# Kernel optimization log

Measured on AMD Instinct MI355X. Metric: run time of the kernel, lower is better.

The kernel has to match this reference:

```python
import jax, jax.numpy as jnp
import numpy as np

E = 512   # embed_dim
H = 8     # num_heads
DH = E // H  # head_dim = 64
L = 1024  # tgt_len (language tokens)
S = 1024  # src_len (video/audio tokens)
B = 8     # batch
EPS = 1e-8


def setup_inputs() -> dict:
    key = jax.random.key(0)
    ks = jax.random.split(key, 12)
    xavier = float(np.sqrt(2.0 / (E + E)))
    inp = {
        "query": jax.random.normal(ks[0], (L, B, E), jnp.float32),
        "mod1": jax.random.normal(ks[1], (S, B, E), jnp.float32),
        "mod2": jax.random.normal(ks[2], (S, B, E), jnp.float32),
    }
    wnames = ["Wq", "Wk1", "Wk2", "Wv1", "Wv2", "Wg1", "Wg2", "Wo"]
    for i, n in enumerate(wnames):
        inp[n] = jax.random.normal(ks[3 + i], (E, E), jnp.float32) * xavier
        inp["b" + n[1:]] = jnp.zeros((E,), jnp.float32)
    return inp


def _heads(x):
    # (T, B, E) -> (B*H, T, DH), fairseq-style head split
    T = x.shape[0]
    return x.reshape(T, B * H, DH).transpose(1, 0, 2)


def reference(query, mod1, mod2,
              Wq, bq, Wk1, bk1, Wk2, bk2,
              Wv1, bv1, Wv2, bv2,
              Wg1, bg1, Wg2, bg2, Wo, bo):
    scaling = DH ** -0.5
    q = (query @ Wq.T + bq) * scaling          # (L, B, E)
    k1 = mod1 @ Wk1.T + bk1                    # (S, B, E)
    k2 = mod2 @ Wk2.T + bk2
    # gated values: v_i * sigmoid(gate_i(mod_i)), summed across modalities
    v = ((mod1 @ Wv1.T + bv1) * jax.nn.sigmoid(mod1 @ Wg1.T + bg1)
         + (mod2 @ Wv2.T + bv2) * jax.nn.sigmoid(mod2 @ Wg2.T + bg2))

    qh, k1h, k2h, vh = _heads(q), _heads(k1), _heads(k2), _heads(v)  # (B*H, T, DH)

    # 3x3 Gram determinant scores (computed via GEMMs, no [B,L,S,D] broadcast)
    ll = jnp.sum(qh * qh, -1)[:, :, None]        # (BH, L, 1)
    vv = jnp.sum(k1h * k1h, -1)[:, None, :]      # (BH, 1, S)
    aa = jnp.sum(k2h * k2h, -1)[:, None, :]
    va = jnp.sum(k1h * k2h, -1)[:, None, :]
    lv = jnp.einsum('bld,bsd->bls', qh, k1h)     # (BH, L, S)
    la = jnp.einsum('bld,bsd->bls', qh, k2h)
    det = (ll * (vv * aa - va * va)
           - lv * (lv * aa - la * va)
           + la * (lv * va - la * vv))
    scores = -jnp.sqrt(jnp.clip(det, EPS))       # (BH, L, S)

    attn = jax.nn.softmax(scores, axis=-1)
    out = jnp.einsum('bls,bsd->bld', attn, vh)   # (BH, L, DH)
    out = out.transpose(1, 0, 2).reshape(L, B, E)
    return out @ Wo.T + bo                       # (L, B, E)
```

## Files before the change

kernel.cpp:

```cpp
#include <hip/hip_runtime.h>
#include <math.h>


typedef short bf16x8 __attribute__((ext_vector_type(8)));
typedef float f32x4  __attribute__((ext_vector_type(4)));

#define MFMA16(a,b,c) __builtin_amdgcn_mfma_f32_16x16x32_bf16((a),(b),(c),0,0,0)

static constexpr float LOG2E_F = 1.4426950408889634f;
static constexpr float CBRT_L2E = 1.12994722f;
static constexpr float DEFER_THR = 11.54156033f;
static constexpr float EPS_SCALED = 2.0813689e-8f;

typedef const __attribute__((address_space(1))) unsigned int gas_u32;
typedef __attribute__((address_space(3))) unsigned int las_u32;

__device__ __forceinline__ void gload16(const void* g, void* l){
  __builtin_amdgcn_global_load_lds((gas_u32*)g, (las_u32*)l, 16, 0, 0);
}

__device__ __forceinline__ float b2f(unsigned short s){
  union { unsigned u; float f; } v; v.u = ((unsigned)s) << 16; return v.f;
}
__device__ __forceinline__ unsigned short f2b(float f){
  union { float f; unsigned u; } v; v.f = f;
  unsigned r = v.u + 0x7fffu + ((v.u >> 16) & 1u);
  return (unsigned short)(r >> 16);
}

__global__ __launch_bounds__(256) void split3_kernel(
    const float* __restrict__ a, const float* __restrict__ b,
    const float* __restrict__ c,
    unsigned short* __restrict__ hi, unsigned short* __restrict__ lo, int n)
{
  const int y = blockIdx.y;
  const float* src = (y == 0) ? a : ((y == 1) ? b : c);
  unsigned short* h = hi + (size_t)y * n;
  unsigned short* L = lo + (size_t)y * n;
  int stride = gridDim.x * 256;
  for (int i = blockIdx.x*256 + threadIdx.x; i < n; i += stride){
    float v = src[i];
    unsigned short hh = f2b(v);
    h[i] = hh;
    L[i] = f2b(v - b2f(hh));
  }
}

__global__ __launch_bounds__(256) void splitW_kernel(
    const float* w0, const float* w1, const float* w2, const float* w3,
    const float* w4, const float* w5, const float* w6, const float* w7,
    unsigned short* __restrict__ hi, unsigned short* __restrict__ lo, int n)
{
  const int y = blockIdx.y;
  const float* src = w0;
  if (y == 1) src = w1; if (y == 2) src = w2; if (y == 3) src = w3;
  if (y == 4) src = w4; if (y == 5) src = w5; if (y == 6) src = w6;
  if (y == 7) src = w7;
  unsigned short* h = hi + (size_t)y * n;
  unsigned short* L = lo + (size_t)y * n;
  int stride = gridDim.x * 256;
  for (int i = blockIdx.x*256 + threadIdx.x; i < n; i += stride){
    float v = src[i];
    unsigned short hh = f2b(v);
    h[i] = hh;
    L[i] = f2b(v - b2f(hh));
  }
}

__global__ __launch_bounds__(256,2) void proj_kernel(
    const unsigned short* __restrict__ xhi, const unsigned short* __restrict__ xlo,
    const unsigned short* __restrict__ whi, const unsigned short* __restrict__ wlo,
    const float* __restrict__ bq, const float* __restrict__ bk1,
    const float* __restrict__ bk2,
    const float* __restrict__ bv1, const float* __restrict__ bg1,
    const float* __restrict__ bv2, const float* __restrict__ bg2,
    unsigned short* __restrict__ qh_hi, unsigned short* __restrict__ qh_lo,
    unsigned short* __restrict__ k1h_hi, unsigned short* __restrict__ k1h_lo,
    unsigned short* __restrict__ k2h_hi, unsigned short* __restrict__ k2h_lo,
    float* __restrict__ vacc1, float* __restrict__ vacc2)
{
  __shared__ unsigned short smem[2*4*4096];
  const int tid = threadIdx.x, w = tid >> 6, l = tid & 63;
  const int y = blockIdx.y;
  const int job = y >> 2;
  const int r0 = blockIdx.x * 128, e0 = (y & 3) * 128;
  const int lrow = l & 15, kg = l >> 4;
  const bool isGate = (job >= 3);

  const size_t NXs = (size_t)8192*512, NWs = (size_t)512*512;
  const int aidx = (job == 0) ? 0 : ((job == 1 || job == 3) ? 1 : 2);
  const unsigned short* Ahi = xhi + (size_t)aidx * NXs;
  const unsigned short* Alo = xlo + (size_t)aidx * NXs;
  const int bidx = isGate ? ((job == 3) ? 3 : 4) : job;
  const unsigned short* Bhi = whi + (size_t)bidx * NWs;
  const unsigned short* Blo = wlo + (size_t)bidx * NWs;
  const unsigned short* Bg  = whi + (size_t)((job == 3) ? 5 : 6) * NWs;

  f32x4 acc[4][4], gacc[4][4];
  #pragma unroll
  for (int m = 0; m < 4; ++m)
    #pragma unroll
    for (int n = 0; n < 4; ++n){
      acc[m][n] = (f32x4){0.f,0.f,0.f,0.f};
      gacc[m][n] = (f32x4){0.f,0.f,0.f,0.f};
    }

  const int sgsw = ((l & 3) ^ ((l >> 3) & 3)) * 8;
  const int srA = r0 + w*16 + (l >> 2);
  const int srB = e0 + w*16 + (l >> 2);

  auto stage = [&](int buf, int kk){
    const int lb = buf*4*4096 + w*512;
    #pragma unroll
    for (int j = 0; j < 2; ++j){
      const size_t ga = (size_t)(srA + j*64)*512 + kk + sgsw;
      const size_t gb = (size_t)(srB + j*64)*512 + kk + sgsw;
      gload16(&Ahi[ga], &smem[lb + 0*4096 + j*2048]);
      if (!isGate) gload16(&Alo[ga], &smem[lb + 1*4096 + j*2048]);
      else         gload16(&Bg[gb],  &smem[lb + 1*4096 + j*2048]);
      gload16(&Bhi[gb], &smem[lb + 2*4096 + j*2048]);
      gload16(&Blo[gb], &smem[lb + 3*4096 + j*2048]);
    }
  };

  const int rowA = (w >> 1)*64 + lrow;
  const int rowB = (w & 1)*64 + lrow;
  const int kgs  = (kg ^ ((lrow >> 1) & 3)) * 8;

  auto compute = [&](int buf){
    const int bb = buf*4*4096;
    bf16x8 ah[4], al[4];
    #pragma unroll
    for (int m = 0; m < 4; ++m){
      const int ra = (rowA + m*16)*32 + kgs;
      ah[m] = *(const bf16x8*)&smem[bb + ra];
      if (!isGate) al[m] = *(const bf16x8*)&smem[bb + 4096 + ra];
    }
    #pragma unroll
    for (int n = 0; n < 4; ++n){
      const int rb = (rowB + n*16)*32 + kgs;
      bf16x8 bh = *(const bf16x8*)&smem[bb + 8192 + rb];
      bf16x8 bl = *(const bf16x8*)&smem[bb + 12288 + rb];
      #pragma unroll
      for (int m = 0; m < 4; ++m){
        acc[m][n] = MFMA16(ah[m], bh, acc[m][n]);
        acc[m][n] = MFMA16(ah[m], bl, acc[m][n]);
      }
      if (!isGate){
        #pragma unroll
        for (int m = 0; m < 4; ++m)
          acc[m][n] = MFMA16(al[m], bh, acc[m][n]);
      } else {
        bf16x8 bg = *(const bf16x8*)&smem[bb + 4096 + rb];
        #pragma unroll
        for (int m = 0; m < 4; ++m)
          gacc[m][n] = MFMA16(ah[m], bg, gacc[m][n]);
      }
    }
  };

  stage(0, 0);
  __syncthreads();
  for (int t = 0; t < 16; ++t){
    if (t < 15) stage((t+1) & 1, (t+1)*32);
    compute(t & 1);
    __syncthreads();
  }

  if (!isGate){
    const float* bias = (job == 0) ? bq : ((job == 1) ? bk1 : bk2);
    const float scale = (job == 0) ? 0.125f*CBRT_L2E : CBRT_L2E;
    unsigned short* oH = (job == 0) ? qh_hi : ((job == 1) ? k1h_hi : k2h_hi);
    unsigned short* oL = (job == 0) ? qh_lo : ((job == 1) ? k1h_lo : k2h_lo);
    #pragma unroll
    for (int n = 0; n < 4; ++n){
      const int e = e0 + (w & 1)*64 + n*16 + lrow;
      const float bv = bias[e];
      #pragma unroll
      for (int m = 0; m < 4; ++m){
        #pragma unroll
        for (int q = 0; q < 4; ++q){
          const int r = r0 + (w >> 1)*64 + m*16 + kg*4 + q;
          const float yv = (acc[m][n][q] + bv) * scale;
          const int bh = ((r & 7) << 3) + (e >> 6);
          const size_t off = ((size_t)bh*1024 + (r >> 3))*64 + (e & 63);
          unsigned short hh = f2b(yv);
          oH[off] = hh;
          oL[off] = f2b(yv - b2f(hh));
        }
      }
    }
  } else {
    const float* bvv = (job == 3) ? bv1 : bv2;
    const float* bgg = (job == 3) ? bg1 : bg2;
    float* outF = (job == 3) ? vacc1 : vacc2;
    #pragma unroll
    for (int n = 0; n < 4; ++n){
      const int e = e0 + (w & 1)*64 + n*16 + lrow;
      const float bv = bvv[e], bg_ = bgg[e];
      #pragma unroll
      for (int m = 0; m < 4; ++m){
        #pragma unroll
        for (int q = 0; q < 4; ++q){
          const int r = r0 + (w >> 1)*64 + m*16 + kg*4 + q;
          const float yv = acc[m][n][q] + bv;
          const float yg = gacc[m][n][q] + bg_;
          const float sg = 1.0f / (1.0f + exp2f(-yg * LOG2E_F));
          outF[(size_t)r*512 + e] = yv * sg;
        }
      }
    }
  }
}

__global__ __launch_bounds__(256,2) void gemmout_kernel(
    const unsigned short* __restrict__ Ahi,
    const unsigned short* __restrict__ Bhi, const unsigned short* __restrict__ Blo,
    const float* __restrict__ bias, float* __restrict__ outF)
{
  __shared__ unsigned short smem[2*10240];
  const int tid = threadIdx.x, w = tid >> 6, l = tid & 63;
  const int r0 = blockIdx.x * 64, e0 = blockIdx.y * 128;
  const int lrow = l & 15, kg = l >> 4;

  f32x4 acc[2][4];
  #pragma unroll
  for (int m = 0; m < 2; ++m)
    #pragma unroll
    for (int n = 0; n < 4; ++n) acc[m][n] = (f32x4){0.f,0.f,0.f,0.f};

  const int sgsw = ((l & 3) ^ ((l >> 3) & 3)) * 8;
  const int srA = r0 + w*16 + (l >> 2);
  const int srB = e0 + w*16 + (l >> 2);

  auto stage = [&](int buf, int kk){
    const int lb = buf*10240;
    gload16(&Ahi[(size_t)srA*512 + kk + sgsw], &smem[lb + tid*8]);
    #pragma unroll
    for (int j = 0; j < 2; ++j){
      const size_t gb = (size_t)(srB + j*64)*512 + kk + sgsw;
      gload16(&Bhi[gb], &smem[lb + 2048 + (tid + j*256)*8]);
      gload16(&Blo[gb], &smem[lb + 6144 + (tid + j*256)*8]);
    }
  };

  const int rowA = (w >> 1)*32 + lrow;
  const int rowB = (w & 1)*64 + lrow;
  const int kgs  = (kg ^ ((lrow >> 1) & 3)) * 8;

  auto compute = [&](int buf){
    const int bb = buf*10240;
    bf16x8 ah[2];
    #pragma unroll
    for (int m = 0; m < 2; ++m)
      ah[m] = *(const bf16x8*)&smem[bb + (rowA + m*16)*32 + kgs];
    #pragma unroll
    for (int n = 0; n < 4; ++n){
      const int rb = (rowB + n*16)*32 + kgs;
      bf16x8 bh = *(const bf16x8*)&smem[bb + 2048 + rb];
      bf16x8 bl = *(const bf16x8*)&smem[bb + 6144 + rb];
      #pragma unroll
      for (int m = 0; m < 2; ++m){
        acc[m][n] = MFMA16(ah[m], bh, acc[m][n]);
        acc[m][n] = MFMA16(ah[m], bl, acc[m][n]);
      }
    }
  };

  stage(0, 0);
  __syncthreads();
  for (int t = 0; t < 16; ++t){
    if (t < 15) stage((t+1) & 1, (t+1)*32);
    compute(t & 1);
    __syncthreads();
  }

  #pragma unroll
  for (int n = 0; n < 4; ++n){
    const int e = e0 + (w & 1)*64 + n*16 + lrow;
    const float bv = bias[e];
    #pragma unroll
    for (int m = 0; m < 2; ++m){
      #pragma unroll
      for (int q = 0; q < 4; ++q){
        const int r = r0 + (w >> 1)*32 + m*16 + kg*4 + q;
        outF[(size_t)r*512 + e] = acc[m][n][q] + bv;
      }
    }
  }
}

__global__ __launch_bounds__(256) void norms_kernel(
    const unsigned short* __restrict__ qh, const unsigned short* __restrict__ ql,
    const unsigned short* __restrict__ k1h, const unsigned short* __restrict__ k1l,
    const unsigned short* __restrict__ k2h, const unsigned short* __restrict__ k2l,
    float* __restrict__ ll, f32x4* __restrict__ nrm4)
{
  const int idx = blockIdx.x*256 + threadIdx.x;
  const size_t base = (size_t)idx * 64;
  float sll = 0.f, svv = 0.f, saa = 0.f, sva = 0.f;
  #pragma unroll
  for (int j = 0; j < 8; ++j){
    bf16x8 q_h = *(const bf16x8*)&qh[base + j*8];
    bf16x8 q_l = *(const bf16x8*)&ql[base + j*8];
    bf16x8 a_h = *(const bf16x8*)&k1h[base + j*8];
    bf16x8 a_l = *(const bf16x8*)&k1l[base + j*8];
    bf16x8 c_h = *(const bf16x8*)&k2h[base + j*8];
    bf16x8 c_l = *(const bf16x8*)&k2l[base + j*8];
    #pragma unroll
    for (int i = 0; i < 8; ++i){
      float qv = b2f((unsigned short)q_h[i]) + b2f((unsigned short)q_l[i]);
      float a1 = b2f((unsigned short)a_h[i]) + b2f((unsigned short)a_l[i]);
      float a2 = b2f((unsigned short)c_h[i]) + b2f((unsigned short)c_l[i]);
      sll += qv*qv; svv += a1*a1; saa += a2*a2; sva += a1*a2;
    }
  }
  ll[idx] = sll;
  nrm4[idx] = (f32x4){svv*saa - sva*sva, saa, 2.0f*sva, svv};
}

__global__ __launch_bounds__(256) void vtrans_kernel(
    const float* __restrict__ v1, const float* __restrict__ v2,
    unsigned short* __restrict__ vTh)
{
  __shared__ unsigned short sH[64*64];
  const int bh = blockIdx.y, b = bh >> 3, h = bh & 7;
  const int s0 = blockIdx.x * 64;
  const int tid = threadIdx.x;
  for (int c = tid; c < 1024; c += 256){
    const int i = c >> 4, sl = c & 15;
    const size_t g = ((size_t)(s0 + i)*8 + b)*512 + h*64 + sl*4;
    f32x4 a = *(const f32x4*)&v1[g];
    f32x4 bb = *(const f32x4*)&v2[g];
    #pragma unroll
    for (int e = 0; e < 4; ++e)
      sH[(sl*4 + e)*64 + i] = f2b(a[e] + bb[e]);
  }
  __syncthreads();
  for (int c = tid; c < 512; c += 256){
    const int d = c >> 3, sl = c & 7;
    const size_t g = ((size_t)bh*64 + d)*1024 + s0 + sl*8;
    *(bf16x8*)&vTh[g] = *(const bf16x8*)&sH[d*64 + sl*8];
  }
}

__global__ __launch_bounds__(256,2) void attn_kernel(
    const unsigned short* __restrict__ qhh, const unsigned short* __restrict__ qhl,
    const unsigned short* __restrict__ k1hh, const unsigned short* __restrict__ k1hl,
    const unsigned short* __restrict__ k2hh, const unsigned short* __restrict__ k2hl,
    const unsigned short* __restrict__ vTh,
    const float* __restrict__ llv, const f32x4* __restrict__ nrm4,
    unsigned short* __restrict__ aoHi)
{
  __shared__ unsigned short sK1h[4096];
  __shared__ unsigned short sK1l[4096];
  __shared__ unsigned short sK2h[4096];
  __shared__ unsigned short sK2l[4096];
  __shared__ unsigned short sVh[4096];
  __shared__ unsigned short sPh[8192];
  __shared__ f32x4 sN4[64];

  const int bh = blockIdx.x & 63, l0 = (blockIdx.x >> 6) * 128;
  const int tid = threadIdx.x, w = tid >> 6, lane = tid & 63;
  const int lrow = lane & 15, kg = lane >> 4;

  bf16x8 qfh[2][2], qfl[2][2];
  #pragma unroll
  for (int m = 0; m < 2; ++m){
    const size_t qb = ((size_t)bh*1024 + l0 + w*32 + m*16 + lrow)*64 + kg*8;
    qfh[m][0] = *(const bf16x8*)&qhh[qb];
    qfl[m][0] = *(const bf16x8*)&qhl[qb];
    qfh[m][1] = *(const bf16x8*)&qhh[qb + 32];
    qfl[m][1] = *(const bf16x8*)&qhl[qb + 32];
  }
  float ll_r[2][4];
  #pragma unroll
  for (int m = 0; m < 2; ++m)
    #pragma unroll
    for (int q = 0; q < 4; ++q)
      ll_r[m][q] = llv[bh*1024 + l0 + w*32 + m*16 + kg*4 + q];

  f32x4 accO[2][4];
  #pragma unroll
  for (int m = 0; m < 2; ++m)
    #pragma unroll
    for (int i = 0; i < 4; ++i) accO[m][i] = (f32x4){0.f,0.f,0.f,0.f};
  float mn[2][4], s_run[2][4];
  #pragma unroll
  for (int m = 0; m < 2; ++m)
    #pragma unroll
    for (int q = 0; q < 4; ++q){ mn[m][q] = 1e30f; s_run[m][q] = 0.f; }

  const int c0 = tid, c1 = tid + 256;
  const int r0g = c0 >> 3, g0 = ((c0 & 7) ^ (r0g & 7)) * 8;
  const int r1g = c1 >> 3, g1 = ((c1 & 7) ^ (r1g & 7)) * 8;

  for (int ss = 0; ss < 1024; ss += 64){
    {
      const size_t kb = (size_t)bh*1024 + ss;
      const size_t k0 = (kb + r0g)*64 + g0;
      const size_t k1_ = (kb + r1g)*64 + g1;
      gload16(&k1hh[k0], &sK1h[c0*8]);  gload16(&k1hh[k1_], &sK1h[c1*8]);
      gload16(&k1hl[k0], &sK1l[c0*8]);  gload16(&k1hl[k1_], &sK1l[c1*8]);
      gload16(&k2hh[k0], &sK2h[c0*8]);  gload16(&k2hh[k1_], &sK2h[c1*8]);
      gload16(&k2hl[k0], &sK2l[c0*8]);  gload16(&k2hl[k1_], &sK2l[c1*8]);
      const size_t v0 = ((size_t)bh*64 + r0g)*1024 + ss + g0;
      const size_t v1 = ((size_t)bh*64 + r1g)*1024 + ss + g1;
      gload16(&vTh[v0], &sVh[c0*8]);    gload16(&vTh[v1], &sVh[c1*8]);
      if (tid < 64) gload16(&nrm4[(size_t)bh*1024 + ss + tid], &sN4[tid]);
    }
    __syncthreads();

    float p_[2][4][4];
    float tmn[2][4];
    #pragma unroll
    for (int m = 0; m < 2; ++m)
      #pragma unroll
      for (int q = 0; q < 4; ++q) tmn[m][q] = 1e30f;

    #pragma unroll
    for (int nt = 0; nt < 4; ++nt){
      f32x4 lv[2], la[2];
      #pragma unroll
      for (int m = 0; m < 2; ++m){ lv[m] = (f32x4){0.f,0.f,0.f,0.f}; la[m] = (f32x4){0.f,0.f,0.f,0.f}; }
      #pragma unroll
      for (int ks = 0; ks < 2; ++ks){
        const int row = nt*16 + lrow;
        const int off = row*64 + (((ks*4 + kg) ^ (row & 7)) * 8);
        bf16x8 b1h = *(const bf16x8*)&sK1h[off];
        bf16x8 b1l = *(const bf16x8*)&sK1l[off];
        bf16x8 b2h = *(const bf16x8*)&sK2h[off];
        bf16x8 b2l = *(const bf16x8*)&sK2l[off];
        #pragma unroll
        for (int m = 0; m < 2; ++m){
          lv[m] = MFMA16(qfh[m][ks], b1h, lv[m]);
          lv[m] = MFMA16(qfh[m][ks], b1l, lv[m]);
          lv[m] = MFMA16(qfl[m][ks], b1h, lv[m]);
          la[m] = MFMA16(qfh[m][ks], b2h, la[m]);
          la[m] = MFMA16(qfh[m][ks], b2l, la[m]);
          la[m] = MFMA16(qfl[m][ks], b2h, la[m]);
        }
      }
      f32x4 n4 = sN4[nt*16 + lrow];
      const float cross = n4[0], c_aa = n4[1], c_va2 = n4[2], c_vv = n4[3];
      #pragma unroll
      for (int m = 0; m < 2; ++m){
        #pragma unroll
        for (int q = 0; q < 4; ++q){
          const float flv = lv[m][q], fla = la[m][q];
          float t = fmaf(-c_vv, fla*fla, (flv*fla)*c_va2);
          t = fmaf(-c_aa, flv*flv, t);
          const float det = fmaf(ll_r[m][q], cross, t);
          const float sq = __builtin_amdgcn_sqrtf(fmaxf(det, EPS_SCALED));
          p_[m][nt][q] = sq;
          tmn[m][q] = fminf(tmn[m][q], sq);
        }
      }
    }
    #pragma unroll
    for (int m = 0; m < 2; ++m)
      #pragma unroll
      for (int q = 0; q < 4; ++q){
        tmn[m][q] = fminf(tmn[m][q], __shfl_xor(tmn[m][q], 1));
        tmn[m][q] = fminf(tmn[m][q], __shfl_xor(tmn[m][q], 2));
        tmn[m][q] = fminf(tmn[m][q], __shfl_xor(tmn[m][q], 4));
        tmn[m][q] = fminf(tmn[m][q], __shfl_xor(tmn[m][q], 8));
      }
    int up = 0;
    #pragma unroll
    for (int m = 0; m < 2; ++m)
      #pragma unroll
      for (int q = 0; q < 4; ++q) up |= (tmn[m][q] < mn[m][q] - DEFER_THR) ? 1 : 0;
    if (__any(up)){
      #pragma unroll
      for (int m = 0; m < 2; ++m)
        #pragma unroll
        for (int q = 0; q < 4; ++q){
          const float mnn = fminf(mn[m][q], tmn[m][q]);
          const float rs = __builtin_amdgcn_exp2f(mnn - mn[m][q]);
          mn[m][q] = mnn;
          s_run[m][q] *= rs;
          #pragma unroll
          for (int dt = 0; dt < 4; ++dt) accO[m][dt][q] *= rs;
        }
    }
    float ps[2][4];
    #pragma unroll
    for (int m = 0; m < 2; ++m)
      #pragma unroll
      for (int q = 0; q < 4; ++q) ps[m][q] = 0.f;
    #pragma unroll
    for (int nt = 0; nt < 4; ++nt)
      #pragma unroll
      for (int m = 0; m < 2; ++m)
        #pragma unroll
        for (int q = 0; q < 4; ++q){
          const float e = __builtin_amdgcn_exp2f(mn[m][q] - p_[m][nt][q]);
          p_[m][nt][q] = e;
          ps[m][q] += e;
        }
    #pragma unroll
    for (int m = 0; m < 2; ++m)
      #pragma unroll
      for (int q = 0; q < 4; ++q){
        float v = ps[m][q];
        v += __shfl_xor(v, 1); v += __shfl_xor(v, 2);
        v += __shfl_xor(v, 4); v += __shfl_xor(v, 8);
        s_run[m][q] += v;
      }

    #pragma unroll
    for (int m = 0; m < 2; ++m){
      #pragma unroll
      for (int nt = 0; nt < 4; ++nt){
        const int col = nt*16 + lrow;
        const int cg = col >> 3, cr = col & 7;
        #pragma unroll
        for (int qp = 0; qp < 2; ++qp){
          unsigned int pk;
          asm("v_cvt_pk_bf16_f32 %0, %1, %2" : "=v"(pk)
              : "v"(p_[m][nt][qp*2]), "v"(p_[m][nt][qp*2+1]));
          const int ra = m*16 + kg*4 + qp*2, rb = ra + 1;
          sPh[w*2048 + ra*64 + ((cg ^ (ra & 7))*8) + cr] = (unsigned short)(pk & 0xffffu);
          sPh[w*2048 + rb*64 + ((cg ^ (rb & 7))*8) + cr] = (unsigned short)(pk >> 16);
        }
      }
    }

    #pragma unroll
    for (int ks = 0; ks < 2; ++ks){
      bf16x8 pa[2];
      #pragma unroll
      for (int m = 0; m < 2; ++m){
        const int prow = m*16 + lrow;
        pa[m] = *(const bf16x8*)&sPh[w*2048 + prow*64 + (((ks*4 + kg) ^ (prow & 7))*8)];
      }
      #pragma unroll
      for (int dt = 0; dt < 4; ++dt){
        const int vrow = dt*16 + lrow;
        bf16x8 bvh = *(const bf16x8*)&sVh[vrow*64 + (((ks*4 + kg) ^ (vrow & 7))*8)];
        #pragma unroll
        for (int m = 0; m < 2; ++m)
          accO[m][dt] = MFMA16(pa[m], bvh, accO[m][dt]);
      }
    }
    __syncthreads();
  }

  const int b = bh >> 3, h = bh & 7;
  #pragma unroll
  for (int m = 0; m < 2; ++m){
    float rcp[4];
    #pragma unroll
    for (int q = 0; q < 4; ++q) rcp[q] = __builtin_amdgcn_rcpf(s_run[m][q]);
    #pragma unroll
    for (int dt = 0; dt < 4; ++dt){
      const int d = dt*16 + lrow;
      #pragma unroll
      for (int q = 0; q < 4; ++q){
        const int l_ = l0 + w*32 + m*16 + kg*4 + q;
        aoHi[((size_t)l_*8 + b)*512 + h*64 + d] = f2b(accO[m][dt][q] * rcp[q]);
      }
    }
  }
}

extern "C" void kernel_launch(void* const* d_in, const int* in_sizes, int n_in,
                              void* d_out, int out_size, void* d_ws, size_t ws_size,
                              hipStream_t stream)
{
  const float* query = (const float*)d_in[0];
  const float* mod1  = (const float*)d_in[1];
  const float* mod2  = (const float*)d_in[2];
  const float* bq  = (const float*)d_in[4];
  const float* bk1 = (const float*)d_in[6];
  const float* bk2 = (const float*)d_in[8];
  const float* bv1 = (const float*)d_in[10];
  const float* bv2 = (const float*)d_in[12];
  const float* bg1 = (const float*)d_in[14];
  const float* bg2 = (const float*)d_in[16];
  const float* bo  = (const float*)d_in[18];

  char* p = (char*)d_ws;
  auto take = [&](size_t bytes) -> char* {
    char* r = p; p += (bytes + 255) & ~(size_t)255; return r;
  };
  const size_t NX = (size_t)8192*512;
  const size_t NW = (size_t)512*512;
  const size_t XB = NX*2, WB = NW*2;
  const size_t HB = (size_t)64*1024*64*2;
  const size_t FB = NX*4;
  const size_t NB = (size_t)64*1024*4;

  unsigned short* xhi = (unsigned short*)take(3*XB);
  unsigned short* xlo = (unsigned short*)take(3*XB);
  unsigned short* whi = (unsigned short*)take(8*WB);
  unsigned short* wlo = (unsigned short*)take(8*WB);
  unsigned short* qh_hi  = (unsigned short*)take(HB);
  unsigned short* qh_lo  = (unsigned short*)take(HB);
  unsigned short* k1h_hi = (unsigned short*)take(HB);
  unsigned short* k1h_lo = (unsigned short*)take(HB);
  unsigned short* k2h_hi = (unsigned short*)take(HB);
  unsigned short* k2h_lo = (unsigned short*)take(HB);
  unsigned short* vT_hi  = (unsigned short*)take(HB);
  float* vacc1 = (float*)take(FB);
  float* vacc2 = (float*)take(FB);
  unsigned short* ao_hi = (unsigned short*)take(HB);
  float* llv = (float*)take(NB);
  f32x4* nrm4 = (f32x4*)take(4*NB);

  split3_kernel<<<dim3(1024,3), 256, 0, stream>>>(query, mod1, mod2, xhi, xlo, (int)NX);
  splitW_kernel<<<dim3(256,8), 256, 0, stream>>>(
      (const float*)d_in[3], (const float*)d_in[5], (const float*)d_in[7],
      (const float*)d_in[9], (const float*)d_in[11], (const float*)d_in[13],
      (const float*)d_in[15], (const float*)d_in[17], whi, wlo, (int)NW);

  proj_kernel<<<dim3(64, 20), 256, 0, stream>>>(
      xhi, xlo, whi, wlo, bq, bk1, bk2, bv1, bg1, bv2, bg2,
      qh_hi, qh_lo, k1h_hi, k1h_lo, k2h_hi, k2h_lo, vacc1, vacc2);

  norms_kernel<<<256, 256, 0, stream>>>(qh_hi, qh_lo, k1h_hi, k1h_lo,
                                        k2h_hi, k2h_lo, llv, nrm4);
  vtrans_kernel<<<dim3(16, 64), 256, 0, stream>>>(vacc1, vacc2, vT_hi);

  attn_kernel<<<512, 256, 0, stream>>>(
      qh_hi, qh_lo, k1h_hi, k1h_lo, k2h_hi, k2h_lo, vT_hi,
      llv, nrm4, ao_hi);

  gemmout_kernel<<<dim3(128, 4), 256, 0, stream>>>(
      ao_hi, whi + 7*NW, wlo + 7*NW, bo, (float*)d_out);
}
```

Measured before the change: 371.0 us.

## Drop activation lo-split in projections, split QK/VG kernels, raise MFMA priority

```diff
diff --git a/kernel.cpp b/kernel.cpp
--- a/kernel.cpp
+++ b/kernel.cpp
@@ -28,21 +28,25 @@
   return (unsigned short)(r >> 16);
 }
 
-__global__ __launch_bounds__(256) void split3_kernel(
+__global__ __launch_bounds__(256) void cast3_kernel(
     const float* __restrict__ a, const float* __restrict__ b,
-    const float* __restrict__ c,
-    unsigned short* __restrict__ hi, unsigned short* __restrict__ lo, int n)
+    const float* __restrict__ c, unsigned short* __restrict__ hi, int n)
 {
   const int y = blockIdx.y;
   const float* src = (y == 0) ? a : ((y == 1) ? b : c);
   unsigned short* h = hi + (size_t)y * n;
-  unsigned short* L = lo + (size_t)y * n;
+  const int n8 = n >> 3;
   int stride = gridDim.x * 256;
-  for (int i = blockIdx.x*256 + threadIdx.x; i < n; i += stride){
-    float v = src[i];
-    unsigned short hh = f2b(v);
-    h[i] = hh;
-    L[i] = f2b(v - b2f(hh));
+  for (int i = blockIdx.x*256 + threadIdx.x; i < n8; i += stride){
+    f32x4 v0 = *(const f32x4*)&src[i*8];
+    f32x4 v1 = *(const f32x4*)&src[i*8 + 4];
+    bf16x8 o;
+    #pragma unroll
+    for (int j = 0; j < 4; ++j){
+      o[j]   = (short)f2b(v0[j]);
+      o[j+4] = (short)f2b(v1[j]);
+    }
+    *(bf16x8*)&h[i*8] = o;
   }
 }
 
@@ -67,59 +71,45 @@
   }
 }
 
-__global__ __launch_bounds__(256,2) void proj_kernel(
-    const unsigned short* __restrict__ xhi, const unsigned short* __restrict__ xlo,
+__global__ __launch_bounds__(256,3) void proj_qk_kernel(
+    const unsigned short* __restrict__ xhi,
     const unsigned short* __restrict__ whi, const unsigned short* __restrict__ wlo,
     const float* __restrict__ bq, const float* __restrict__ bk1,
     const float* __restrict__ bk2,
-    const float* __restrict__ bv1, const float* __restrict__ bg1,
-    const float* __restrict__ bv2, const float* __restrict__ bg2,
     unsigned short* __restrict__ qh_hi, unsigned short* __restrict__ qh_lo,
     unsigned short* __restrict__ k1h_hi, unsigned short* __restrict__ k1h_lo,
-    unsigned short* __restrict__ k2h_hi, unsigned short* __restrict__ k2h_lo,
-    float* __restrict__ vacc1, float* __restrict__ vacc2)
-{
-  __shared__ unsigned short smem[2*4*4096];
+    unsigned short* __restrict__ k2h_hi, unsigned short* __restrict__ k2h_lo)
+{
+  __shared__ unsigned short smem[2*3*4096];
   const int tid = threadIdx.x, w = tid >> 6, l = tid & 63;
-  const int y = blockIdx.y;
-  const int job = y >> 2;
+  const int y = blockIdx.y, job = y >> 2;
   const int r0 = blockIdx.x * 128, e0 = (y & 3) * 128;
   const int lrow = l & 15, kg = l >> 4;
-  const bool isGate = (job >= 3);
 
   const size_t NXs = (size_t)8192*512, NWs = (size_t)512*512;
-  const int aidx = (job == 0) ? 0 : ((job == 1 || job == 3) ? 1 : 2);
-  const unsigned short* Ahi = xhi + (size_t)aidx * NXs;
-  const unsigned short* Alo = xlo + (size_t)aidx * NXs;
-  const int bidx = isGate ? ((job == 3) ? 3 : 4) : job;
-  const unsigned short* Bhi = whi + (size_t)bidx * NWs;
-  const unsigned short* Blo = wlo + (size_t)bidx * NWs;
-  const unsigned short* Bg  = whi + (size_t)((job == 3) ? 5 : 6) * NWs;
-
-  f32x4 acc[4][4], gacc[4][4];
+  const unsigned short* Ahi = xhi + (size_t)job * NXs;
+  const unsigned short* B1  = whi + (size_t)job * NWs;
+  const unsigned short* B2  = wlo + (size_t)job * NWs;
+
+  f32x4 acc[4][4];
   #pragma unroll
   for (int m = 0; m < 4; ++m)
     #pragma unroll
-    for (int n = 0; n < 4; ++n){
-      acc[m][n] = (f32x4){0.f,0.f,0.f,0.f};
-      gacc[m][n] = (f32x4){0.f,0.f,0.f,0.f};
-    }
+    for (int n = 0; n < 4; ++n) acc[m][n] = (f32x4){0.f,0.f,0.f,0.f};
 
   const int sgsw = ((l & 3) ^ ((l >> 3) & 3)) * 8;
   const int srA = r0 + w*16 + (l >> 2);
   const int srB = e0 + w*16 + (l >> 2);
 
   auto stage = [&](int buf, int kk){
-    const int lb = buf*4*4096 + w*512;
+    const int lb = buf*3*4096 + w*512;
     #pragma unroll
     for (int j = 0; j < 2; ++j){
       const size_t ga = (size_t)(srA + j*64)*512 + kk + sgsw;
       const size_t gb = (size_t)(srB + j*64)*512 + kk + sgsw;
-      gload16(&Ahi[ga], &smem[lb + 0*4096 + j*2048]);
-      if (!isGate) gload16(&Alo[ga], &smem[lb + 1*4096 + j*2048]);
-      else         gload16(&Bg[gb],  &smem[lb + 1*4096 + j*2048]);
-      gload16(&Bhi[gb], &smem[lb + 2*4096 + j*2048]);
-      gload16(&Blo[gb], &smem[lb + 3*4096 + j*2048]);
+      gload16(&Ahi[ga], &smem[lb + 0    + j*2048]);
+      gload16(&B1[gb],  &smem[lb + 4096 + j*2048]);
+      gload16(&B2[gb],  &smem[lb + 8192 + j*2048]);
     }
   };
 
@@ -128,33 +118,20 @@
   const int kgs  = (kg ^ ((lrow >> 1) & 3)) * 8;
 
   auto compute = [&](int buf){
-    const int bb = buf*4*4096;
-    bf16x8 ah[4], al[4];
-    #pragma unroll
-    for (int m = 0; m < 4; ++m){
-      const int ra = (rowA + m*16)*32 + kgs;
-      ah[m] = *(const bf16x8*)&smem[bb + ra];
-      if (!isGate) al[m] = *(const bf16x8*)&smem[bb + 4096 + ra];
-    }
+    const int bb = buf*3*4096;
+    bf16x8 ah[4];
+    #pragma unroll
+    for (int m = 0; m < 4; ++m)
+      ah[m] = *(const bf16x8*)&smem[bb + (rowA + m*16)*32 + kgs];
     #pragma unroll
     for (int n = 0; n < 4; ++n){
       const int rb = (rowB + n*16)*32 + kgs;
-      bf16x8 bh = *(const bf16x8*)&smem[bb + 8192 + rb];
-      bf16x8 bl = *(const bf16x8*)&smem[bb + 12288 + rb];
+      bf16x8 b1 = *(const bf16x8*)&smem[bb + 4096 + rb];
+      bf16x8 b2 = *(const bf16x8*)&smem[bb + 8192 + rb];
       #pragma unroll
       for (int m = 0; m < 4; ++m){
-        acc[m][n] = MFMA16(ah[m], bh, acc[m][n]);
-        acc[m][n] = MFMA16(ah[m], bl, acc[m][n]);
-      }
-      if (!isGate){
-        #pragma unroll
-        for (int m = 0; m < 4; ++m)
-          acc[m][n] = MFMA16(al[m], bh, acc[m][n]);
-      } else {
-        bf16x8 bg = *(const bf16x8*)&smem[bb + 4096 + rb];
-        #pragma unroll
-        for (int m = 0; m < 4; ++m)
-          gacc[m][n] = MFMA16(ah[m], bg, gacc[m][n]);
+        acc[m][n] = MFMA16(ah[m], b1, acc[m][n]);
+        acc[m][n] = MFMA16(ah[m], b2, acc[m][n]);
       }
     }
   };
@@ -167,47 +144,120 @@
     __syncthreads();
   }
 
-  if (!isGate){
-    const float* bias = (job == 0) ? bq : ((job == 1) ? bk1 : bk2);
-    const float scale = (job == 0) ? 0.125f*CBRT_L2E : CBRT_L2E;
-    unsigned short* oH = (job == 0) ? qh_hi : ((job == 1) ? k1h_hi : k2h_hi);
-    unsigned short* oL = (job == 0) ? qh_lo : ((job == 1) ? k1h_lo : k2h_lo);
+  const float* bias = (job == 0) ? bq : ((job == 1) ? bk1 : bk2);
+  const float scale = (job == 0) ? 0.125f*CBRT_L2E : CBRT_L2E;
+  unsigned short* oH = (job == 0) ? qh_hi : ((job == 1) ? k1h_hi : k2h_hi);
+  unsigned short* oL = (job == 0) ? qh_lo : ((job == 1) ? k1h_lo : k2h_lo);
+  #pragma unroll
+  for (int n = 0; n < 4; ++n){
+    const int e = e0 + (w & 1)*64 + n*16 + lrow;
+    const float bv = bias[e];
+    #pragma unroll
+    for (int m = 0; m < 4; ++m){
+      #pragma unroll
+      for (int q = 0; q < 4; ++q){
+        const int r = r0 + (w >> 1)*64 + m*16 + kg*4 + q;
+        const float yv = (acc[m][n][q] + bv) * scale;
+        const int bh = ((r & 7) << 3) + (e >> 6);
+        const size_t off = ((size_t)bh*1024 + (r >> 3))*64 + (e & 63);
+        unsigned short hh = f2b(yv);
+        oH[off] = hh;
+        oL[off] = f2b(yv - b2f(hh));
+      }
+    }
+  }
+}
+
+__global__ __launch_bounds__(256,2) void proj_vg_kernel(
+    const unsigned short* __restrict__ xhi,
+    const unsigned short* __restrict__ whi,
+    const float* __restrict__ bv1, const float* __restrict__ bg1,
+    const float* __restrict__ bv2, const float* __restrict__ bg2,
+    float* __restrict__ vacc1, float* __restrict__ vacc2)
+{
+  __shared__ unsigned short smem[2*3*4096];
+  const int tid = threadIdx.x, w = tid >> 6, l = tid & 63;
+  const int y = blockIdx.y, job = 3 + (y >> 2);
+  const int r0 = blockIdx.x * 128, e0 = (y & 3) * 128;
+  const int lrow = l & 15, kg = l >> 4;
+
+  const size_t NXs = (size_t)8192*512, NWs = (size_t)512*512;
+  const unsigned short* Ahi = xhi + (size_t)(job - 2) * NXs;
+  const unsigned short* B1  = whi + (size_t)((job == 3) ? 3 : 4) * NWs;
+  const unsigned short* B2  = whi + (size_t)((job == 3) ? 5 : 6) * NWs;
+
+  f32x4 acc[4][4], acc2[4][4];
+  #pragma unroll
+  for (int m = 0; m < 4; ++m)
     #pragma unroll
     for (int n = 0; n < 4; ++n){
-      const int e = e0 + (w & 1)*64 + n*16 + lrow;
-      const float bv = bias[e];
+      acc[m][n] = (f32x4){0.f,0.f,0.f,0.f};
+      acc2[m][n] = (f32x4){0.f,0.f,0.f,0.f};
+    }
+
+  const int sgsw = ((l & 3) ^ ((l >> 3) & 3)) * 8;
+  const int srA = r0 + w*16 + (l >> 2);
+  const int srB = e0 + w*16 + (l >> 2);
+
+  auto stage = [&](int buf, int kk){
+    const int lb = buf*3*4096 + w*512;
+    #pragma unroll
+    for (int j = 0; j < 2; ++j){
+      const size_t ga = (size_t)(srA + j*64)*512 + kk + sgsw;
+      const size_t gb = (size_t)(srB + j*64)*512 + kk + sgsw;
+      gload16(&Ahi[ga], &smem[lb + 0    + j*2048]);
+      gload16(&B1[gb],  &smem[lb + 4096 + j*2048]);
+      gload16(&B2[gb],  &smem[lb + 8192 + j*2048]);
+    }
+  };
+
+  const int rowA = (w >> 1)*64 + lrow;
+  const int rowB = (w & 1)*64 + lrow;
+  const int kgs  = (kg ^ ((lrow >> 1) & 3)) * 8;
+
+  auto compute = [&](int buf){
+    const int bb = buf*3*4096;
+    bf16x8 ah[4];
+    #pragma unroll
+    for (int m = 0; m < 4; ++m)
+      ah[m] = *(const bf16x8*)&smem[bb + (rowA + m*16)*32 + kgs];
+    #pragma unroll
+    for (int n = 0; n < 4; ++n){
+      const int rb = (rowB + n*16)*32 + kgs;
+      bf16x8 b1 = *(const bf16x8*)&smem[bb + 4096 + rb];
+      bf16x8 b2 = *(const bf16x8*)&smem[bb + 8192 + rb];
       #pragma unroll
       for (int m = 0; m < 4; ++m){
-        #pragma unroll
-        for (int q = 0; q < 4; ++q){
-          const int r = r0 + (w >> 1)*64 + m*16 + kg*4 + q;
-          const float yv = (acc[m][n][q] + bv) * scale;
-          const int bh = ((r & 7) << 3) + (e >> 6);
-          const size_t off = ((size_t)bh*1024 + (r >> 3))*64 + (e & 63);
-          unsigned short hh = f2b(yv);
-          oH[off] = hh;
-          oL[off] = f2b(yv - b2f(hh));
-        }
-      }
-    }
-  } else {
-    const float* bvv = (job == 3) ? bv1 : bv2;
-    const float* bgg = (job == 3) ? bg1 : bg2;
-    float* outF = (job == 3) ? vacc1 : vacc2;
-    #pragma unroll
-    for (int n = 0; n < 4; ++n){
-      const int e = e0 + (w & 1)*64 + n*16 + lrow;
-      const float bv = bvv[e], bg_ = bgg[e];
-      #pragma unroll
-      for (int m = 0; m < 4; ++m){
-        #pragma unroll
-        for (int q = 0; q < 4; ++q){
-          const int r = r0 + (w >> 1)*64 + m*16 + kg*4 + q;
-          const float yv = acc[m][n][q] + bv;
-          const float yg = gacc[m][n][q] + bg_;
-          const float sg = 1.0f / (1.0f + exp2f(-yg * LOG2E_F));
-          outF[(size_t)r*512 + e] = yv * sg;
-        }
+        acc[m][n]  = MFMA16(ah[m], b1, acc[m][n]);
+        acc2[m][n] = MFMA16(ah[m], b2, acc2[m][n]);
+      }
+    }
+  };
+
+  stage(0, 0);
+  __syncthreads();
+  for (int t = 0; t < 16; ++t){
+    if (t < 15) stage((t+1) & 1, (t+1)*32);
+    compute(t & 1);
+    __syncthreads();
+  }
+
+  const float* bvv = (job == 3) ? bv1 : bv2;
+  const float* bgg = (job == 3) ? bg1 : bg2;
+  float* outF = (job == 3) ? vacc1 : vacc2;
+  #pragma unroll
+  for (int n = 0; n < 4; ++n){
+    const int e = e0 + (w & 1)*64 + n*16 + lrow;
+    const float bv = bvv[e], bg_ = bgg[e];
+    #pragma unroll
+    for (int m = 0; m < 4; ++m){
+      #pragma unroll
+      for (int q = 0; q < 4; ++q){
+        const int r = r0 + (w >> 1)*64 + m*16 + kg*4 + q;
+        const float yv = acc[m][n][q] + bv;
+        const float yg = acc2[m][n][q] + bg_;
+        const float sg = 1.0f / (1.0f + exp2f(-yg * LOG2E_F));
+        outF[(size_t)r*512 + e] = yv * sg;
       }
     }
   }
@@ -423,6 +473,7 @@
       f32x4 lv[2], la[2];
       #pragma unroll
       for (int m = 0; m < 2; ++m){ lv[m] = (f32x4){0.f,0.f,0.f,0.f}; la[m] = (f32x4){0.f,0.f,0.f,0.f}; }
+      __builtin_amdgcn_s_setprio(1);
       #pragma unroll
       for (int ks = 0; ks < 2; ++ks){
         const int row = nt*16 + lrow;
@@ -441,6 +492,7 @@
           la[m] = MFMA16(qfl[m][ks], b2h, la[m]);
         }
       }
+      __builtin_amdgcn_s_setprio(0);
       f32x4 n4 = sN4[nt*16 + lrow];
       const float cross = n4[0], c_aa = n4[1], c_va2 = n4[2], c_vv = n4[3];
       #pragma unroll
@@ -527,6 +579,7 @@
       }
     }
 
+    __builtin_amdgcn_s_setprio(1);
     #pragma unroll
     for (int ks = 0; ks < 2; ++ks){
       bf16x8 pa[2];
@@ -544,6 +597,7 @@
           accO[m][dt] = MFMA16(pa[m], bvh, accO[m][dt]);
       }
     }
+    __builtin_amdgcn_s_setprio(0);
     __syncthreads();
   }
 
@@ -593,7 +647,6 @@
   const size_t NB = (size_t)64*1024*4;
 
   unsigned short* xhi = (unsigned short*)take(3*XB);
-  unsigned short* xlo = (unsigned short*)take(3*XB);
   unsigned short* whi = (unsigned short*)take(8*WB);
   unsigned short* wlo = (unsigned short*)take(8*WB);
   unsigned short* qh_hi  = (unsigned short*)take(HB);
@@ -609,15 +662,17 @@
   float* llv = (float*)take(NB);
   f32x4* nrm4 = (f32x4*)take(4*NB);
 
-  split3_kernel<<<dim3(1024,3), 256, 0, stream>>>(query, mod1, mod2, xhi, xlo, (int)NX);
+  cast3_kernel<<<dim3(2048,3), 256, 0, stream>>>(query, mod1, mod2, xhi, (int)NX);
   splitW_kernel<<<dim3(256,8), 256, 0, stream>>>(
       (const float*)d_in[3], (const float*)d_in[5], (const float*)d_in[7],
       (const float*)d_in[9], (const float*)d_in[11], (const float*)d_in[13],
       (const float*)d_in[15], (const float*)d_in[17], whi, wlo, (int)NW);
 
-  proj_kernel<<<dim3(64, 20), 256, 0, stream>>>(
-      xhi, xlo, whi, wlo, bq, bk1, bk2, bv1, bg1, bv2, bg2,
-      qh_hi, qh_lo, k1h_hi, k1h_lo, k2h_hi, k2h_lo, vacc1, vacc2);
+  proj_qk_kernel<<<dim3(64, 12), 256, 0, stream>>>(
+      xhi, whi, wlo, bq, bk1, bk2,
+      qh_hi, qh_lo, k1h_hi, k1h_lo, k2h_hi, k2h_lo);
+  proj_vg_kernel<<<dim3(64, 8), 256, 0, stream>>>(
+      xhi, whi, bv1, bg1, bv2, bg2, vacc1, vacc2);
 
   norms_kernel<<<256, 256, 0, stream>>>(qh_hi, qh_lo, k1h_hi, k1h_lo,
                                         k2h_hi, k2h_lo, llv, nrm4);
```

Measured after the change: 349.9 us. -5.7%, faster.
